# Optimization experiments

Hardware: AMD Instinct MI355X
Metric: run time of the kernel (lower is better)

Reference implementation:

```python
import jax, jax.numpy as jnp
import numpy as np

N, E = 50000, 800000
IN_DIM, HEADS, OUT_DIM = 256, 8, 32
NEG_SLOPE = 0.2  # PyG GATConv default leaky_relu slope
LN_EPS = 1e-5


def setup_inputs() -> dict:
    key = jax.random.key(0)
    ks = jax.random.split(key, 8)
    HC = HEADS * OUT_DIM
    x = jax.random.normal(ks[0], (N, IN_DIM), dtype=jnp.float32)
    edge_index = jax.random.randint(ks[1], (2, E), 0, N, dtype=jnp.int32)
    # GATConv params: lin (no bias), att_src/att_dst [H,C], output bias [H*C]
    W = jax.random.normal(ks[2], (IN_DIM, HC), dtype=jnp.float32) / np.sqrt(IN_DIM)
    att_src = jax.random.normal(ks[3], (HEADS, OUT_DIM), dtype=jnp.float32) / np.sqrt(OUT_DIM)
    att_dst = jax.random.normal(ks[4], (HEADS, OUT_DIM), dtype=jnp.float32) / np.sqrt(OUT_DIM)
    bias = jnp.zeros((HC,), dtype=jnp.float32)
    ln_gamma = jnp.ones((HC,), dtype=jnp.float32)
    ln_beta = jnp.zeros((HC,), dtype=jnp.float32)
    return {"x": x, "edge_index": edge_index, "W": W, "att_src": att_src,
            "att_dst": att_dst, "bias": bias, "ln_gamma": ln_gamma, "ln_beta": ln_beta}


def reference(x, edge_index, W, att_src, att_dst, bias, ln_gamma, ln_beta):
    n = x.shape[0]
    # GATConv adds self-loops by default
    loop = jnp.arange(n, dtype=edge_index.dtype)
    src = jnp.concatenate([edge_index[0], loop])  # [E+N]
    dst = jnp.concatenate([edge_index[1], loop])
    h = (x @ W).reshape(n, HEADS, OUT_DIM)              # [N,H,C]
    a_src = jnp.einsum('nhc,hc->nh', h, att_src)        # [N,H]
    a_dst = jnp.einsum('nhc,hc->nh', h, att_dst)
    e = jax.nn.leaky_relu(a_src[src] + a_dst[dst], NEG_SLOPE)  # [E+N,H]
    # segment-softmax over incoming edges of each destination node
    m = jax.ops.segment_max(e, dst, num_segments=n)
    e = jnp.exp(e - m[dst])
    denom = jax.ops.segment_sum(e, dst, num_segments=n)
    alpha = e / (denom[dst] + 1e-16)                    # [E+N,H]
    out = jax.ops.segment_sum(h[src] * alpha[:, :, None], dst, num_segments=n)
    out = out.reshape(n, HEADS * OUT_DIM) + bias        # concat heads + bias
    # LayerNorm(out_dim*heads); dropout is identity in eval
    mu = jnp.mean(out, axis=-1, keepdims=True)
    var = jnp.mean(jnp.square(out - mu), axis=-1, keepdims=True)
    return ln_gamma * (out - mu) * jax.lax.rsqrt(var + LN_EPS) + ln_beta
```

## Files before the change

kernel.cpp:

```cpp
#include <hip/hip_runtime.h>
#include <hip/hip_bf16.h>

#define HEADS 8
#define OUT_DIM 32
#define HC 256
#define IN_DIM 256
#define NEG_SLOPE 0.2f
#define LN_EPS 1e-5f
#define CAP 64

typedef __attribute__((ext_vector_type(8))) short bf16x8;
typedef __attribute__((ext_vector_type(4))) float f32x4;
typedef __attribute__((ext_vector_type(2))) float f32x2;

__device__ __forceinline__ unsigned short f2bf(float f) {
    unsigned int u = __float_as_uint(f);
    unsigned int r = u + 0x7FFFu + ((u >> 16) & 1u);
    return (unsigned short)(r >> 16);
}
__device__ __forceinline__ unsigned short f2bf_hw(float f) {
    union { __hip_bfloat16 h; unsigned short u; } c;
    c.h = __float2bfloat16(f);
    return c.u;
}
__device__ __forceinline__ bf16x8 pack8(const float4 a, const float4 b) {
    bf16x8 r;
    r[0] = (short)f2bf_hw(a.x); r[1] = (short)f2bf_hw(a.y);
    r[2] = (short)f2bf_hw(a.z); r[3] = (short)f2bf_hw(a.w);
    r[4] = (short)f2bf_hw(b.x); r[5] = (short)f2bf_hw(b.y);
    r[6] = (short)f2bf_hw(b.z); r[7] = (short)f2bf_hw(b.w);
    return r;
}

__global__ __launch_bounds__(256) void prep0(const float* __restrict__ W,
                                             unsigned short* __restrict__ Wt,
                                             const float* __restrict__ X,
                                             unsigned short* __restrict__ Xb,
                                             int* __restrict__ cnt,
                                             int N, int nXb) {
    const int b = blockIdx.x;
    const int t = threadIdx.x;
    if (b < 16) {
        __shared__ float tile[64][65];
        const int n0 = (b & 3) * 64;
        const int k0 = (b >> 2) * 64;
        const int r = t >> 4;
        const int c = (t & 15) * 4;
#pragma unroll
        for (int j = 0; j < 4; j++) {
            const int kl = r + j * 16;
            const float4 v = *(const float4*)(W + (size_t)(k0 + kl) * HC + n0 + c);
            tile[kl][c + 0] = v.x; tile[kl][c + 1] = v.y;
            tile[kl][c + 2] = v.z; tile[kl][c + 3] = v.w;
        }
        __syncthreads();
#pragma unroll
        for (int j = 0; j < 4; j++) {
            const int nr = r + j * 16;
            ushort4 o;
            o.x = f2bf(tile[c + 0][nr]);
            o.y = f2bf(tile[c + 1][nr]);
            o.z = f2bf(tile[c + 2][nr]);
            o.w = f2bf(tile[c + 3][nr]);
            *(ushort4*)(Wt + (size_t)(n0 + nr) * IN_DIM + k0 + c) = o;
        }
    } else if (b < 16 + nXb) {
        const size_t i = ((size_t)(b - 16) * 256 + t) * 8;
        if (i < (size_t)N * IN_DIM) {
            const float4 v0 = *(const float4*)(X + i);
            const float4 v1 = *(const float4*)(X + i + 4);
            *(bf16x8*)(Xb + i) = pack8(v0, v1);
        }
    } else {
        const int idx = (b - 16 - nXb) * 256 + t;
        if (idx < N) cnt[idx] = 0;
    }
}

__global__ __launch_bounds__(256) void gemm_sc(const unsigned short* __restrict__ Xb,
                                               const unsigned short* __restrict__ Wt,
                                               unsigned short* __restrict__ Hb,
                                               const float* __restrict__ att_s,
                                               const float* __restrict__ att_d,
                                               float* __restrict__ a_s,
                                               float* __restrict__ a_d,
                                               const int* __restrict__ ei,
                                               int* __restrict__ cnt,
                                               unsigned short* __restrict__ bucket,
                                               int E, int N) {
    const int b = blockIdx.x;
    const int t = threadIdx.x;
    const int nTiles = (N + 63) >> 6;
    const int nSc = (E + N + 511) >> 9;
    const int g = b >> 1;

    if (!(b & 1) && g < nTiles) {
        const int w = t >> 6, lane = t & 63;
        const int l16 = lane & 15, quad = lane >> 4;
        const int m0 = g * 64;
        const int n0 = w * 64;

        const unsigned short* ap[4];
#pragma unroll
        for (int mi = 0; mi < 4; mi++) {
            const int gm = m0 + mi * 16 + l16;
            ap[mi] = Xb + (size_t)(gm < N ? gm : 0) * IN_DIM + quad * 8;
        }
        const unsigned short* bp[4];
#pragma unroll
        for (int ni = 0; ni < 4; ni++)
            bp[ni] = Wt + (size_t)(n0 + ni * 16 + l16) * IN_DIM + quad * 8;

        f32x4 acc[4][4] = {};
#pragma unroll
        for (int k0 = 0; k0 < IN_DIM; k0 += 32) {
            bf16x8 af[4], bfr[4];
#pragma unroll
            for (int mi = 0; mi < 4; mi++) af[mi]  = *(const bf16x8*)(ap[mi] + k0);
#pragma unroll
            for (int ni = 0; ni < 4; ni++) bfr[ni] = *(const bf16x8*)(bp[ni] + k0);
#pragma unroll
            for (int ni = 0; ni < 4; ni++)
#pragma unroll
                for (int mi = 0; mi < 4; mi++)
                    acc[mi][ni] = __builtin_amdgcn_mfma_f32_16x16x32_bf16(af[mi], bfr[ni], acc[mi][ni], 0, 0, 0);
        }

        {
            float as_v[4], ad_v[4];
#pragma unroll
            for (int ni = 0; ni < 4; ni++) {
                as_v[ni] = att_s[n0 + ni * 16 + l16];
                ad_v[ni] = att_d[n0 + ni * 16 + l16];
            }
#pragma unroll
            for (int mi = 0; mi < 4; mi++) {
#pragma unroll
                for (int reg = 0; reg < 4; reg++) {
                    float ps0 = acc[mi][0][reg] * as_v[0] + acc[mi][1][reg] * as_v[1];
                    float ps1 = acc[mi][2][reg] * as_v[2] + acc[mi][3][reg] * as_v[3];
                    float pd0 = acc[mi][0][reg] * ad_v[0] + acc[mi][1][reg] * ad_v[1];
                    float pd1 = acc[mi][2][reg] * ad_v[2] + acc[mi][3][reg] * ad_v[3];
#pragma unroll
                    for (int m = 1; m <= 2; m <<= 1) {
                        ps0 += __shfl_xor(ps0, m); ps1 += __shfl_xor(ps1, m);
                        pd0 += __shfl_xor(pd0, m); pd1 += __shfl_xor(pd1, m);
                    }
                    const int s2 = l16 & 3;
                    float v = s2 == 0 ? ps0 : (s2 == 1 ? ps1 : (s2 == 2 ? pd0 : pd1));
                    v += __shfl_xor(v, 4); v += __shfl_xor(v, 8);
                    const int gm = m0 + mi * 16 + quad * 4 + reg;
                    if (l16 < 4 && gm < N) {
                        float* dst = (l16 >= 2) ? a_d : a_s;
                        dst[(size_t)gm * HEADS + 2 * w + (l16 & 1)] = v;
                    }
                }
            }
        }

#pragma unroll
        for (int mi = 0; mi < 4; mi++) {
#pragma unroll
            for (int reg = 0; reg < 4; reg++) {
                const int gm = m0 + mi * 16 + quad * 4 + reg;
                if (gm < N) {
#pragma unroll
                    for (int ni = 0; ni < 4; ni++)
                        Hb[(size_t)gm * HC + n0 + ni * 16 + l16] = f2bf_hw(acc[mi][ni][reg]);
                }
            }
        }
    } else {
        const int sc = b - min((b + 1) >> 1, nTiles);
        if (sc >= nSc) return;
        const int ebase = sc << 9;
#pragma unroll
        for (int r = 0; r < 2; r++) {
            const int e = ebase + (r << 8) + t;
            if (e < E + N) {
                int s, d;
                if (e < E) { s = ei[e]; d = ei[E + e]; }
                else       { s = d = e - E; }
                int slot = atomicAdd(&cnt[d], 1);
                if (slot < CAP) bucket[(size_t)d * CAP + slot] = (unsigned short)s;
            }
        }
    }
}

__global__ __launch_bounds__(256) void csr_agg(const int* __restrict__ cntArr,
                                               const unsigned short* __restrict__ bucket,
                                               const unsigned short* __restrict__ Hb,
                                               const float* __restrict__ a_s,
                                               const float* __restrict__ a_d,
                                               const float* __restrict__ bias,
                                               const float* __restrict__ gamma,
                                               const float* __restrict__ beta,
                                               float* __restrict__ out, int N) {
    const int lane = threadIdx.x & 63;
    const int node = blockIdx.x * 4 + (threadIdx.x >> 6);
    if (node >= N) return;
    const int half = lane >> 5;
    const int sl   = lane & 31;
    const int c0   = sl * 8;
    const int hh   = sl >> 2;
    const size_t base = (size_t)node * CAP;
    const int cnt  = min(cntArr[node], CAP);
    const float adv = a_d[(size_t)node * HEADS + hh];
    const int breg = (int)bucket[base + lane];

    f32x2 acc2[4] = {};
    float wsum = 0.f;
    const int nIter = (cnt + 7) >> 3;

    float tl[4]; float msk[4]; uint4 hv[4];
#pragma unroll
    for (int j = 0; j < 4; j++) {
        const int idx = 2 * j + half;
        const int s = __shfl(breg, idx);
        const bool ok = idx < cnt;
        const int sv = ok ? s : 0;
        msk[j] = ok ? 1.f : 0.f;
        tl[j] = a_s[(size_t)sv * HEADS + hh];
        hv[j] = *(const uint4*)(Hb + (size_t)sv * HC + c0);
    }

    for (int it = 0; it < nIter; ++it) {
        float tl2[4]; float msk2[4]; uint4 hv2[4];
        const int i2 = (it + 1) * 8;
#pragma unroll
        for (int j = 0; j < 4; j++) {
            const int idx = i2 + 2 * j + half;
            const int s = __shfl(breg, idx & 63);
            const bool ok = idx < cnt;
            const int sv = ok ? s : 0;
            msk2[j] = ok ? 1.f : 0.f;
            tl2[j] = a_s[(size_t)sv * HEADS + hh];
            hv2[j] = *(const uint4*)(Hb + (size_t)sv * HC + c0);
        }
#pragma unroll
        for (int j = 0; j < 4; j++) {
            const float tt = tl[j] + adv;
            const float l = fmaxf(tt, NEG_SLOPE * tt);
            const float ww = msk[j] * __expf(l);
            wsum += ww;
            f32x2 wv; wv.x = ww; wv.y = ww;
            f32x2 p0, p1, p2, p3;
            p0.x = __uint_as_float(hv[j].x << 16); p0.y = __uint_as_float(hv[j].x & 0xffff0000u);
            p1.x = __uint_as_float(hv[j].y << 16); p1.y = __uint_as_float(hv[j].y & 0xffff0000u);
            p2.x = __uint_as_float(hv[j].z << 16); p2.y = __uint_as_float(hv[j].z & 0xffff0000u);
            p3.x = __uint_as_float(hv[j].w << 16); p3.y = __uint_as_float(hv[j].w & 0xffff0000u);
            acc2[0] += wv * p0;
            acc2[1] += wv * p1;
            acc2[2] += wv * p2;
            acc2[3] += wv * p3;
        }
#pragma unroll
        for (int j = 0; j < 4; j++) { tl[j] = tl2[j]; msk[j] = msk2[j]; hv[j] = hv2[j]; }
    }

    float acc[8];
    acc[0] = acc2[0].x; acc[1] = acc2[0].y; acc[2] = acc2[1].x; acc[3] = acc2[1].y;
    acc[4] = acc2[2].x; acc[5] = acc2[2].y; acc[6] = acc2[3].x; acc[7] = acc2[3].y;

#pragma unroll
    for (int k = 0; k < 8; k++) acc[k] += __shfl_xor(acc[k], 32);
    wsum += __shfl_xor(wsum, 32);

    const float inv = 1.f / (wsum + 1e-16f);
    const float4 b0 = *(const float4*)(bias + c0);
    const float4 b1 = *(const float4*)(bias + c0 + 4);
    float v[8];
    v[0] = acc[0] * inv + b0.x; v[1] = acc[1] * inv + b0.y;
    v[2] = acc[2] * inv + b0.z; v[3] = acc[3] * inv + b0.w;
    v[4] = acc[4] * inv + b1.x; v[5] = acc[5] * inv + b1.y;
    v[6] = acc[6] * inv + b1.z; v[7] = acc[7] * inv + b1.w;

    float s1 = v[0] + v[1] + v[2] + v[3] + v[4] + v[5] + v[6] + v[7];
#pragma unroll
    for (int m = 1; m < 64; m <<= 1) s1 += __shfl_xor(s1, m);
    const float mu = s1 * (1.f / 512.f);
    float d[8];
    float sq = 0.f;
#pragma unroll
    for (int k = 0; k < 8; k++) { d[k] = v[k] - mu; sq += d[k] * d[k]; }
#pragma unroll
    for (int m = 1; m < 64; m <<= 1) sq += __shfl_xor(sq, m);
    const float rs = rsqrtf(sq * (1.f / 512.f) + LN_EPS);

    const float e0 = half ? d[4] : d[0];
    const float e1 = half ? d[5] : d[1];
    const float e2 = half ? d[6] : d[2];
    const float e3 = half ? d[7] : d[3];
    const int co = c0 + half * 4;
    const float4 g  = *(const float4*)(gamma + co);
    const float4 be = *(const float4*)(beta + co);
    float4 o;
    o.x = g.x * e0 * rs + be.x;
    o.y = g.y * e1 * rs + be.y;
    o.z = g.z * e2 * rs + be.z;
    o.w = g.w * e3 * rs + be.w;
    *(float4*)(out + (size_t)node * HC + co) = o;
}

extern "C" void kernel_launch(void* const* d_in, const int* in_sizes, int n_in,
                              void* d_out, int out_size, void* d_ws, size_t ws_size,
                              hipStream_t stream) {
    const float* x     = (const float*)d_in[0];
    const int*   ei    = (const int*)d_in[1];
    const float* W     = (const float*)d_in[2];
    const float* att_s = (const float*)d_in[3];
    const float* att_d = (const float*)d_in[4];
    const float* bias  = (const float*)d_in[5];
    const float* gamma = (const float*)d_in[6];
    const float* beta  = (const float*)d_in[7];
    float* out = (float*)d_out;

    const int N = in_sizes[0] / IN_DIM;
    const int E = in_sizes[1] / 2;

    unsigned short* Hb = (unsigned short*)d_ws;
    unsigned short* Wt = Hb + (size_t)N * HC;
    unsigned short* Xb = Wt + (size_t)IN_DIM * HC;
    float* a_s  = (float*)(Xb + (size_t)N * IN_DIM);
    float* a_d  = a_s + (size_t)N * HEADS;
    int* cnt    = (int*)(a_d + (size_t)N * HEADS);
    unsigned short* bucket = (unsigned short*)(cnt + N);

    const int nXb = (int)(((size_t)N * IN_DIM / 8 + 255) / 256);
    const int nZe = (N + 255) / 256;
    prep0<<<16 + nXb + nZe, 256, 0, stream>>>(W, Wt, x, Xb, cnt, N, nXb);

    const int nTiles = (N + 63) / 64;
    const int nSc = (E + N + 511) / 512;
    gemm_sc<<<nTiles + nSc, 256, 0, stream>>>(Xb, Wt, Hb, att_s, att_d, a_s, a_d,
                                              ei, cnt, bucket, E, N);

    csr_agg<<<(N + 3) / 4, 256, 0, stream>>>(cnt, bucket, Hb, a_s, a_d,
                                             bias, gamma, beta, out, N);
}
```

Baseline: 250.1 us.

## Convert X to bf16 inside GEMM and pad atomic counters to separate cache lines

The separate pass that converts X to a bf16 buffer is removed. The GEMM now loads fp32 X directly and packs it to bf16 in registers, which avoids writing and then rereading a 25 MB intermediate. The per-node edge counters are also spaced 16 ints apart (64 bytes), so the scatter's atomics on neighbouring nodes no longer hit the same cache line. In exchange, the GEMM's A-operand loads double in size, there is extra conversion ALU work in the inner loop, and the counter array to zero grows sixteenfold.

```diff
diff --git a/kernel.cpp b/kernel.cpp
--- a/kernel.cpp
+++ b/kernel.cpp
@@ -8,6 +8,7 @@
 #define NEG_SLOPE 0.2f
 #define LN_EPS 1e-5f
 #define CAP 64
+#define CSTR 16
 
 typedef __attribute__((ext_vector_type(8))) short bf16x8;
 typedef __attribute__((ext_vector_type(4))) float f32x4;
@@ -34,10 +35,8 @@
 
 __global__ __launch_bounds__(256) void prep0(const float* __restrict__ W,
                                              unsigned short* __restrict__ Wt,
-                                             const float* __restrict__ X,
-                                             unsigned short* __restrict__ Xb,
                                              int* __restrict__ cnt,
-                                             int N, int nXb) {
+                                             int N) {
     const int b = blockIdx.x;
     const int t = threadIdx.x;
     if (b < 16) {
@@ -64,20 +63,14 @@
             o.w = f2bf(tile[c + 3][nr]);
             *(ushort4*)(Wt + (size_t)(n0 + nr) * IN_DIM + k0 + c) = o;
         }
-    } else if (b < 16 + nXb) {
-        const size_t i = ((size_t)(b - 16) * 256 + t) * 8;
-        if (i < (size_t)N * IN_DIM) {
-            const float4 v0 = *(const float4*)(X + i);
-            const float4 v1 = *(const float4*)(X + i + 4);
-            *(bf16x8*)(Xb + i) = pack8(v0, v1);
-        }
     } else {
-        const int idx = (b - 16 - nXb) * 256 + t;
-        if (idx < N) cnt[idx] = 0;
+        const size_t i = ((size_t)(b - 16) * 256 + t) * 4;
+        if (i < (size_t)N * CSTR)
+            *(int4*)(cnt + i) = make_int4(0, 0, 0, 0);
     }
 }
 
-__global__ __launch_bounds__(256) void gemm_sc(const unsigned short* __restrict__ Xb,
+__global__ __launch_bounds__(256) void gemm_sc(const float* __restrict__ X,
                                                const unsigned short* __restrict__ Wt,
                                                unsigned short* __restrict__ Hb,
                                                const float* __restrict__ att_s,
@@ -100,11 +93,11 @@
         const int m0 = g * 64;
         const int n0 = w * 64;
 
-        const unsigned short* ap[4];
+        const float* ap[4];
 #pragma unroll
         for (int mi = 0; mi < 4; mi++) {
             const int gm = m0 + mi * 16 + l16;
-            ap[mi] = Xb + (size_t)(gm < N ? gm : 0) * IN_DIM + quad * 8;
+            ap[mi] = X + (size_t)(gm < N ? gm : 0) * IN_DIM + quad * 8;
         }
         const unsigned short* bp[4];
 #pragma unroll
@@ -116,9 +109,13 @@
         for (int k0 = 0; k0 < IN_DIM; k0 += 32) {
             bf16x8 af[4], bfr[4];
 #pragma unroll
-            for (int mi = 0; mi < 4; mi++) af[mi]  = *(const bf16x8*)(ap[mi] + k0);
-#pragma unroll
             for (int ni = 0; ni < 4; ni++) bfr[ni] = *(const bf16x8*)(bp[ni] + k0);
+#pragma unroll
+            for (int mi = 0; mi < 4; mi++) {
+                const float4 a0 = *(const float4*)(ap[mi] + k0);
+                const float4 a1 = *(const float4*)(ap[mi] + k0 + 4);
+                af[mi] = pack8(a0, a1);
+            }
 #pragma unroll
             for (int ni = 0; ni < 4; ni++)
 #pragma unroll
@@ -181,7 +178,7 @@
                 int s, d;
                 if (e < E) { s = ei[e]; d = ei[E + e]; }
                 else       { s = d = e - E; }
-                int slot = atomicAdd(&cnt[d], 1);
+                int slot = atomicAdd(&cnt[(size_t)d * CSTR], 1);
                 if (slot < CAP) bucket[(size_t)d * CAP + slot] = (unsigned short)s;
             }
         }
@@ -205,7 +202,7 @@
     const int c0   = sl * 8;
     const int hh   = sl >> 2;
     const size_t base = (size_t)node * CAP;
-    const int cnt  = min(cntArr[node], CAP);
+    const int cnt  = min(cntArr[(size_t)node * CSTR], CAP);
     const float adv = a_d[(size_t)node * HEADS + hh];
     const int breg = (int)bucket[base + lane];
 
@@ -321,19 +318,17 @@
 
     unsigned short* Hb = (unsigned short*)d_ws;
     unsigned short* Wt = Hb + (size_t)N * HC;
-    unsigned short* Xb = Wt + (size_t)IN_DIM * HC;
-    float* a_s  = (float*)(Xb + (size_t)N * IN_DIM);
+    float* a_s  = (float*)(Wt + (size_t)IN_DIM * HC);
     float* a_d  = a_s + (size_t)N * HEADS;
     int* cnt    = (int*)(a_d + (size_t)N * HEADS);
-    unsigned short* bucket = (unsigned short*)(cnt + N);
-
-    const int nXb = (int)(((size_t)N * IN_DIM / 8 + 255) / 256);
-    const int nZe = (N + 255) / 256;
-    prep0<<<16 + nXb + nZe, 256, 0, stream>>>(W, Wt, x, Xb, cnt, N, nXb);
+    unsigned short* bucket = (unsigned short*)(cnt + (size_t)N * CSTR);
+
+    const int nZe = (int)(((size_t)N * CSTR / 4 + 255) / 256);
+    prep0<<<16 + nZe, 256, 0, stream>>>(W, Wt, cnt, N);
 
     const int nTiles = (N + 63) / 64;
     const int nSc = (E + N + 511) / 512;
-    gemm_sc<<<nTiles + nSc, 256, 0, stream>>>(Xb, Wt, Hb, att_s, att_d, a_s, a_d,
+    gemm_sc<<<nTiles + nSc, 256, 0, stream>>>(x, Wt, Hb, att_s, att_d, a_s, a_d,
                                               ei, cnt, bucket, E, N);
 
     csr_agg<<<(N + 3) / 4, 256, 0, stream>>>(cnt, bucket, Hb, a_s, a_d,
```

Result: slower. 284.6 us (+13.8%).

## Move edge bucketing into the cast kernel and zero counters with memset

Applied to the files above, without the earlier changes.

The edge scatter (atomic bucketing by destination) moves out of the GEMM kernel and into the prep kernel, where its blocks interleave with the fp32-to-bf16 cast blocks. The GEMM becomes a standalone kernel. Counter zeroing is replaced by a hipMemsetAsync so the counts are cleared before the scatter runs in the prep kernel. The aim is to overlap latency-bound atomics with bandwidth-bound casting instead of with MFMA work, at the cost of an extra memset launch.

```diff
diff --git a/kernel.cpp b/kernel.cpp
--- a/kernel.cpp
+++ b/kernel.cpp
@@ -32,18 +32,42 @@
     return r;
 }
 
-__global__ __launch_bounds__(256) void prep0(const float* __restrict__ W,
-                                             unsigned short* __restrict__ Wt,
-                                             const float* __restrict__ X,
-                                             unsigned short* __restrict__ Xb,
-                                             int* __restrict__ cnt,
-                                             int N, int nXb) {
+__global__ __launch_bounds__(256) void prep_sc(const float* __restrict__ W,
+                                               unsigned short* __restrict__ Wt,
+                                               const float* __restrict__ X,
+                                               unsigned short* __restrict__ Xb,
+                                               const int* __restrict__ ei,
+                                               int* __restrict__ cnt,
+                                               unsigned short* __restrict__ bucket,
+                                               int E, int N, int nSc, int nXb) {
     const int b = blockIdx.x;
     const int t = threadIdx.x;
-    if (b < 16) {
+
+    int castJob = -1, scJob = -1;
+    if (b < 2 * nSc) {
+        if (b & 1) castJob = b >> 1;
+        else       scJob   = b >> 1;
+    } else {
+        castJob = b - nSc;
+    }
+
+    if (scJob >= 0) {
+        const int ebase = scJob << 9;
+#pragma unroll
+        for (int r = 0; r < 2; r++) {
+            const int e = ebase + (r << 8) + t;
+            if (e < E + N) {
+                int s, d;
+                if (e < E) { s = ei[e]; d = ei[E + e]; }
+                else       { s = d = e - E; }
+                int slot = atomicAdd(&cnt[d], 1);
+                if (slot < CAP) bucket[(size_t)d * CAP + slot] = (unsigned short)s;
+            }
+        }
+    } else if (castJob < 16) {
         __shared__ float tile[64][65];
-        const int n0 = (b & 3) * 64;
-        const int k0 = (b >> 2) * 64;
+        const int n0 = (castJob & 3) * 64;
+        const int k0 = (castJob >> 2) * 64;
         const int r = t >> 4;
         const int c = (t & 15) * 4;
 #pragma unroll
@@ -64,125 +88,99 @@
             o.w = f2bf(tile[c + 3][nr]);
             *(ushort4*)(Wt + (size_t)(n0 + nr) * IN_DIM + k0 + c) = o;
         }
-    } else if (b < 16 + nXb) {
-        const size_t i = ((size_t)(b - 16) * 256 + t) * 8;
-        if (i < (size_t)N * IN_DIM) {
-            const float4 v0 = *(const float4*)(X + i);
-            const float4 v1 = *(const float4*)(X + i + 4);
-            *(bf16x8*)(Xb + i) = pack8(v0, v1);
-        }
     } else {
-        const int idx = (b - 16 - nXb) * 256 + t;
-        if (idx < N) cnt[idx] = 0;
-    }
-}
-
-__global__ __launch_bounds__(256) void gemm_sc(const unsigned short* __restrict__ Xb,
-                                               const unsigned short* __restrict__ Wt,
-                                               unsigned short* __restrict__ Hb,
-                                               const float* __restrict__ att_s,
-                                               const float* __restrict__ att_d,
-                                               float* __restrict__ a_s,
-                                               float* __restrict__ a_d,
-                                               const int* __restrict__ ei,
-                                               int* __restrict__ cnt,
-                                               unsigned short* __restrict__ bucket,
-                                               int E, int N) {
-    const int b = blockIdx.x;
+        const int xc = castJob - 16;
+        if (xc < nXb) {
+            const size_t i = ((size_t)xc * 256 + t) * 8;
+            if (i < (size_t)N * IN_DIM) {
+                const float4 v0 = *(const float4*)(X + i);
+                const float4 v1 = *(const float4*)(X + i + 4);
+                *(bf16x8*)(Xb + i) = pack8(v0, v1);
+            }
+        }
+    }
+}
+
+__global__ __launch_bounds__(256) void gemm_bf16(const unsigned short* __restrict__ Xb,
+                                                 const unsigned short* __restrict__ Wt,
+                                                 unsigned short* __restrict__ Hb,
+                                                 const float* __restrict__ att_s,
+                                                 const float* __restrict__ att_d,
+                                                 float* __restrict__ a_s,
+                                                 float* __restrict__ a_d, int N) {
     const int t = threadIdx.x;
-    const int nTiles = (N + 63) >> 6;
-    const int nSc = (E + N + 511) >> 9;
-    const int g = b >> 1;
-
-    if (!(b & 1) && g < nTiles) {
-        const int w = t >> 6, lane = t & 63;
-        const int l16 = lane & 15, quad = lane >> 4;
-        const int m0 = g * 64;
-        const int n0 = w * 64;
-
-        const unsigned short* ap[4];
+    const int w = t >> 6, lane = t & 63;
+    const int l16 = lane & 15, quad = lane >> 4;
+    const int m0 = blockIdx.x * 64;
+    const int n0 = w * 64;
+
+    const unsigned short* ap[4];
+#pragma unroll
+    for (int mi = 0; mi < 4; mi++) {
+        const int gm = m0 + mi * 16 + l16;
+        ap[mi] = Xb + (size_t)(gm < N ? gm : 0) * IN_DIM + quad * 8;
+    }
+    const unsigned short* bp[4];
+#pragma unroll
+    for (int ni = 0; ni < 4; ni++)
+        bp[ni] = Wt + (size_t)(n0 + ni * 16 + l16) * IN_DIM + quad * 8;
+
+    f32x4 acc[4][4] = {};
+#pragma unroll
+    for (int k0 = 0; k0 < IN_DIM; k0 += 32) {
+        bf16x8 af[4], bfr[4];
+#pragma unroll
+        for (int mi = 0; mi < 4; mi++) af[mi]  = *(const bf16x8*)(ap[mi] + k0);
+#pragma unroll
+        for (int ni = 0; ni < 4; ni++) bfr[ni] = *(const bf16x8*)(bp[ni] + k0);
+#pragma unroll
+        for (int ni = 0; ni < 4; ni++)
+#pragma unroll
+            for (int mi = 0; mi < 4; mi++)
+                acc[mi][ni] = __builtin_amdgcn_mfma_f32_16x16x32_bf16(af[mi], bfr[ni], acc[mi][ni], 0, 0, 0);
+    }
+
+    {
+        float as_v[4], ad_v[4];
+#pragma unroll
+        for (int ni = 0; ni < 4; ni++) {
+            as_v[ni] = att_s[n0 + ni * 16 + l16];
+            ad_v[ni] = att_d[n0 + ni * 16 + l16];
+        }
 #pragma unroll
         for (int mi = 0; mi < 4; mi++) {
-            const int gm = m0 + mi * 16 + l16;
-            ap[mi] = Xb + (size_t)(gm < N ? gm : 0) * IN_DIM + quad * 8;
-        }
-        const unsigned short* bp[4];
-#pragma unroll
-        for (int ni = 0; ni < 4; ni++)
-            bp[ni] = Wt + (size_t)(n0 + ni * 16 + l16) * IN_DIM + quad * 8;
-
-        f32x4 acc[4][4] = {};
-#pragma unroll
-        for (int k0 = 0; k0 < IN_DIM; k0 += 32) {
-            bf16x8 af[4], bfr[4];
-#pragma unroll
-            for (int mi = 0; mi < 4; mi++) af[mi]  = *(const bf16x8*)(ap[mi] + k0);
-#pragma unroll
-            for (int ni = 0; ni < 4; ni++) bfr[ni] = *(const bf16x8*)(bp[ni] + k0);
-#pragma unroll
-            for (int ni = 0; ni < 4; ni++)
-#pragma unroll
-                for (int mi = 0; mi < 4; mi++)
-                    acc[mi][ni] = __builtin_amdgcn_mfma_f32_16x16x32_bf16(af[mi], bfr[ni], acc[mi][ni], 0, 0, 0);
-        }
-
-        {
-            float as_v[4], ad_v[4];
-#pragma unroll
-            for (int ni = 0; ni < 4; ni++) {
-                as_v[ni] = att_s[n0 + ni * 16 + l16];
-                ad_v[ni] = att_d[n0 + ni * 16 + l16];
-            }
-#pragma unroll
-            for (int mi = 0; mi < 4; mi++) {
-#pragma unroll
-                for (int reg = 0; reg < 4; reg++) {
-                    float ps0 = acc[mi][0][reg] * as_v[0] + acc[mi][1][reg] * as_v[1];
-                    float ps1 = acc[mi][2][reg] * as_v[2] + acc[mi][3][reg] * as_v[3];
-                    float pd0 = acc[mi][0][reg] * ad_v[0] + acc[mi][1][reg] * ad_v[1];
-                    float pd1 = acc[mi][2][reg] * ad_v[2] + acc[mi][3][reg] * ad_v[3];
-#pragma unroll
-                    for (int m = 1; m <= 2; m <<= 1) {
-                        ps0 += __shfl_xor(ps0, m); ps1 += __shfl_xor(ps1, m);
-                        pd0 += __shfl_xor(pd0, m); pd1 += __shfl_xor(pd1, m);
-                    }
-                    const int s2 = l16 & 3;
-                    float v = s2 == 0 ? ps0 : (s2 == 1 ? ps1 : (s2 == 2 ? pd0 : pd1));
-                    v += __shfl_xor(v, 4); v += __shfl_xor(v, 8);
-                    const int gm = m0 + mi * 16 + quad * 4 + reg;
-                    if (l16 < 4 && gm < N) {
-                        float* dst = (l16 >= 2) ? a_d : a_s;
-                        dst[(size_t)gm * HEADS + 2 * w + (l16 & 1)] = v;
-                    }
+#pragma unroll
+            for (int reg = 0; reg < 4; reg++) {
+                float ps0 = acc[mi][0][reg] * as_v[0] + acc[mi][1][reg] * as_v[1];
+                float ps1 = acc[mi][2][reg] * as_v[2] + acc[mi][3][reg] * as_v[3];
+                float pd0 = acc[mi][0][reg] * ad_v[0] + acc[mi][1][reg] * ad_v[1];
+                float pd1 = acc[mi][2][reg] * ad_v[2] + acc[mi][3][reg] * ad_v[3];
+#pragma unroll
+                for (int m = 1; m <= 2; m <<= 1) {
+                    ps0 += __shfl_xor(ps0, m); ps1 += __shfl_xor(ps1, m);
+                    pd0 += __shfl_xor(pd0, m); pd1 += __shfl_xor(pd1, m);
+                }
+                const int s2 = l16 & 3;
+                float v = s2 == 0 ? ps0 : (s2 == 1 ? ps1 : (s2 == 2 ? pd0 : pd1));
+                v += __shfl_xor(v, 4); v += __shfl_xor(v, 8);
+                const int gm = m0 + mi * 16 + quad * 4 + reg;
+                if (l16 < 4 && gm < N) {
+                    float* dst = (l16 >= 2) ? a_d : a_s;
+                    dst[(size_t)gm * HEADS + 2 * w + (l16 & 1)] = v;
                 }
             }
         }
-
-#pragma unroll
-        for (int mi = 0; mi < 4; mi++) {
-#pragma unroll
-            for (int reg = 0; reg < 4; reg++) {
-                const int gm = m0 + mi * 16 + quad * 4 + reg;
-                if (gm < N) {
-#pragma unroll
-                    for (int ni = 0; ni < 4; ni++)
-                        Hb[(size_t)gm * HC + n0 + ni * 16 + l16] = f2bf_hw(acc[mi][ni][reg]);
-                }
-            }
-        }
-    } else {
-        const int sc = b - min((b + 1) >> 1, nTiles);
-        if (sc >= nSc) return;
-        const int ebase = sc << 9;
-#pragma unroll
-        for (int r = 0; r < 2; r++) {
-            const int e = ebase + (r << 8) + t;
-            if (e < E + N) {
-                int s, d;
-                if (e < E) { s = ei[e]; d = ei[E + e]; }
-                else       { s = d = e - E; }
-                int slot = atomicAdd(&cnt[d], 1);
-                if (slot < CAP) bucket[(size_t)d * CAP + slot] = (unsigned short)s;
+    }
+
+#pragma unroll
+    for (int mi = 0; mi < 4; mi++) {
+#pragma unroll
+        for (int reg = 0; reg < 4; reg++) {
+            const int gm = m0 + mi * 16 + quad * 4 + reg;
+            if (gm < N) {
+#pragma unroll
+                for (int ni = 0; ni < 4; ni++)
+                    Hb[(size_t)gm * HC + n0 + ni * 16 + l16] = f2bf_hw(acc[mi][ni][reg]);
             }
         }
     }
@@ -327,14 +325,16 @@
     int* cnt    = (int*)(a_d + (size_t)N * HEADS);
     unsigned short* bucket = (unsigned short*)(cnt + N);
 
+    hipMemsetAsync(cnt, 0, (size_t)N * sizeof(int), stream);
+
     const int nXb = (int)(((size_t)N * IN_DIM / 8 + 255) / 256);
-    const int nZe = (N + 255) / 256;
-    prep0<<<16 + nXb + nZe, 256, 0, stream>>>(W, Wt, x, Xb, cnt, N, nXb);
-
-    const int nTiles = (N + 63) / 64;
     const int nSc = (E + N + 511) / 512;
-    gemm_sc<<<nTiles + nSc, 256, 0, stream>>>(Xb, Wt, Hb, att_s, att_d, a_s, a_d,
-                                              ei, cnt, bucket, E, N);
+    const int nCast = 16 + nXb;
+    prep_sc<<<nCast + nSc, 256, 0, stream>>>(W, Wt, x, Xb, ei, cnt, bucket,
+                                             E, N, nSc, nXb);
+
+    gemm_bf16<<<(N + 63) / 64, 256, 0, stream>>>(Xb, Wt, Hb, att_s, att_d,
+                                                 a_s, a_d, N);
 
     csr_agg<<<(N + 3) / 4, 256, 0, stream>>>(cnt, bucket, Hb, a_s, a_d,
                                              bias, gamma, beta, out, N);
```

After: 260.4 us. 1.04x slower.
